# Kernel tuning notes

Hardware: AMD Instinct MI355X
Metric: run time of the kernel (lower is better)

Reference implementation:

```python
import jax, jax.numpy as jnp
import numpy as np

GROUPS = 32
EPS = 1e-5


def group_norm(x, gamma, beta):
    B, C, D, H, W = x.shape
    xr = x.reshape(B, GROUPS, C // GROUPS, D, H, W)
    mean = xr.mean(axis=(2, 3, 4, 5), keepdims=True)
    var = xr.var(axis=(2, 3, 4, 5), keepdims=True)
    xn = (xr - mean) * jax.lax.rsqrt(var + EPS)
    xn = xn.reshape(B, C, D, H, W)
    return xn * gamma[None, :, None, None, None] + beta[None, :, None, None, None]


def conv1x1(h, w, b):
    # 1x1x1 Conv3d == channel matmul. w: [O, C], b: [O]
    return jnp.einsum('oc,bcdhw->bodhw', w, h) + b[None, :, None, None, None]


def setup_inputs() -> dict:
    key = jax.random.key(0)
    ks = jax.random.split(key, 10)
    B, C, D, H, W = 2, 128, 16, 16, 16
    x = jax.random.normal(ks[0], (B, C, D, H, W), dtype=jnp.float32)
    gn_w = jnp.ones((C,), dtype=jnp.float32)
    gn_b = jnp.zeros((C,), dtype=jnp.float32)
    # xavier_uniform for [C, C, 1, 1, 1] conv: fan_in = fan_out = C
    lim = float(np.sqrt(6.0 / (C + C)))
    wq = jax.random.uniform(ks[1], (C, C), jnp.float32, -lim, lim)
    wk = jax.random.uniform(ks[2], (C, C), jnp.float32, -lim, lim)
    wv = jax.random.uniform(ks[3], (C, C), jnp.float32, -lim, lim)
    wp = jax.random.uniform(ks[4], (C, C), jnp.float32, -lim, lim) * 1e-05
    bq = jnp.zeros((C,), jnp.float32)
    bk = jnp.zeros((C,), jnp.float32)
    bv = jnp.zeros((C,), jnp.float32)
    bp = jnp.zeros((C,), jnp.float32)
    return {"x": x, "gn_w": gn_w, "gn_b": gn_b, "wq": wq, "bq": bq,
            "wk": wk, "bk": bk, "wv": wv, "bv": bv, "wp": wp, "bp": bp}


def reference(x, gn_w, gn_b, wq, bq, wk, bk, wv, bv, wp, bp):
    B, C, D, H, W = x.shape
    N = D * H * W
    h = group_norm(x, gn_w, gn_b)
    q = conv1x1(h, wq, bq)
    k = conv1x1(h, wk, bk)
    v = conv1x1(h, wv, bv)
    q = q.transpose(0, 2, 3, 4, 1).reshape(B, N, C)   # [B, N, C]
    k = k.reshape(B, C, N)                            # [B, C, N]
    v = v.transpose(0, 2, 3, 4, 1).reshape(B, N, C)   # [B, N, C]
    w = jnp.einsum('bnc,bcm->bnm', q, k) * (C ** -0.5)  # [B, N, N]
    w = jax.nn.softmax(w, axis=-1)
    h = jnp.einsum('bnm,bmc->bnc', w, v)              # [B, N, C]
    h = h.reshape(B, D, H, W, C).transpose(0, 4, 1, 2, 3)
    h = conv1x1(h, wp, bp)
    return x + h
```

## Files before the change

kernel.cpp:

```cpp
#include <hip/hip_runtime.h>
#include <math.h>

#define CC 128
#define NN 4096
#define BB 2
#define NGROUPS 32
#define CPG 4
#define GSIZE (CPG*NN)
#define KSPLIT 8

typedef __attribute__((ext_vector_type(8))) __bf16 bf16x8;
typedef __attribute__((ext_vector_type(4))) float floatx4;

__device__ __forceinline__ unsigned short f2bf(float f) {
  union { float f; unsigned u; } v; v.f = f;
  unsigned r = v.u + 0x7fff + ((v.u >> 16) & 1);
  return (unsigned short)(r >> 16);
}
__device__ __forceinline__ float bf2f(unsigned short u) {
  return __uint_as_float(((unsigned)u) << 16);
}


__device__ __forceinline__ void stage_tile(const unsigned short* __restrict__ gtile,
                                           unsigned short* ltile, int w, int lane) {
  int swl = ((lane >> 2) << 5) | ((((lane & 3) ^ ((lane >> 3) & 3))) << 3);
  #pragma unroll
  for (int j = 0; j < 4; j++) {
    int off = (w*4 + j) * 512;
    __builtin_amdgcn_global_load_lds(
        (const __attribute__((address_space(1))) unsigned int*)(gtile + off + swl),
        (__attribute__((address_space(3))) unsigned int*)(ltile + off),
        16, 0, 0);
  }
}

__global__ void gn_stats_kernel(const float* __restrict__ x, float2* __restrict__ stats,
                                const float* __restrict__ wq, const float* __restrict__ wk,
                                const float* __restrict__ wv, const float* __restrict__ wp,
                                unsigned short* __restrict__ wqb, unsigned short* __restrict__ wkb,
                                unsigned short* __restrict__ wvb, unsigned short* __restrict__ wpb) {
  int t = threadIdx.x;
  if (blockIdx.x < 256) {
    int bid = blockIdx.x;
    const float4* base = (const float4*)(x + (size_t)bid * 4096);
    float4 v = base[t];
    float s  = v.x + v.y + v.z + v.w;
    float ss = v.x*v.x + v.y*v.y + v.z*v.z + v.w*v.w;
    #pragma unroll
    for (int off = 1; off < 64; off <<= 1) {
      s  += __shfl_xor(s, off);
      ss += __shfl_xor(ss, off);
    }
    __shared__ float sred[4], ssred[4];
    if ((t & 63) == 0) { sred[t >> 6] = s; ssred[t >> 6] = ss; }
    __syncthreads();
    if (t == 0)
      stats[bid] = make_float2(sred[0]+sred[1]+sred[2]+sred[3],
                               ssred[0]+ssred[1]+ssred[2]+ssred[3]);
  } else {
    const float sc = 0.08838834764831845f;
    int i = (blockIdx.x - 256) * 256 + t;
    int id = i >> 12, local = i & 4095;
    const float* src = id==0 ? wq : id==1 ? wk : id==2 ? wv : wp;
    unsigned short* dst = id==0 ? wqb : id==1 ? wkb : id==2 ? wvb : wpb;
    float s = (id == 0) ? sc : 1.0f;
    float4 v = ((const float4*)src)[local];
    unsigned p0 = (unsigned)f2bf(v.x*s) | ((unsigned)f2bf(v.y*s) << 16);
    unsigned p1 = (unsigned)f2bf(v.z*s) | ((unsigned)f2bf(v.w*s) << 16);
    ((uint2*)dst)[local] = make_uint2(p0, p1);
  }
}

__global__ __launch_bounds__(256, 2) void qkv_kernel(
    const float* __restrict__ x, const float2* __restrict__ stats,
    const float* __restrict__ gamma, const float* __restrict__ beta,
    const unsigned short* __restrict__ wqb, const unsigned short* __restrict__ wkb,
    const unsigned short* __restrict__ wvb,
    const float* __restrict__ bq, const float* __restrict__ bk, const float* __restrict__ bv,
    unsigned short* __restrict__ q, unsigned short* __restrict__ k, unsigned short* __restrict__ v) {
  int b = blockIdx.y, n0 = blockIdx.x * 16;
  __shared__ unsigned short hs[16][130];
  __shared__ unsigned short vs[16][136];
  __shared__ float gm[NGROUPS], gr[NGROUPS], aa[CC], ab[CC];
  int t = threadIdx.x;
  if (t < NGROUPS) {
    float su = 0.f, ssq = 0.f;
    #pragma unroll
    for (int j = 0; j < 4; j++) {
      float2 p = stats[(b*NGROUPS + t)*4 + j];
      su += p.x; ssq += p.y;
    }
    float mean = su * (1.0f/GSIZE);
    float var  = ssq * (1.0f/GSIZE) - mean*mean;
    gm[t] = mean;
    gr[t] = rsqrtf(var + 1e-5f);
  }
  __syncthreads();
  if (t < CC) {
    int g = t >> 2;
    float a = gr[g] * gamma[t];
    aa[t] = a;
    ab[t] = beta[t] - gm[g] * a;
  }
  __syncthreads();
  #pragma unroll
  for (int j = 0; j < 2; j++) {
    int idx = j*256 + t;
    int c = idx >> 2, n4 = idx & 3;
    float4 xv = *(const float4*)(x + ((size_t)b*CC + c)*NN + n0 + n4*4);
    float a = aa[c], bc = ab[c];
    hs[n4*4+0][c] = f2bf(a*xv.x + bc);
    hs[n4*4+1][c] = f2bf(a*xv.y + bc);
    hs[n4*4+2][c] = f2bf(a*xv.z + bc);
    hs[n4*4+3][c] = f2bf(a*xv.w + bc);
  }
  __syncthreads();
  int w = t >> 6, lane = t & 63, quad = lane >> 4, c = lane & 15;
  int o0 = w * 32;
  bf16x8 af[4];
  #pragma unroll
  for (int ks = 0; ks < 4; ks++)
    af[ks] = *(const bf16x8*)&hs[c][ks*32 + quad*8];
  floatx4 aq[2], ak[2], av[2];
  #pragma unroll
  for (int ct = 0; ct < 2; ct++) {
    aq[ct] = (floatx4){0.f,0.f,0.f,0.f};
    ak[ct] = (floatx4){0.f,0.f,0.f,0.f};
    av[ct] = (floatx4){0.f,0.f,0.f,0.f};
  }
  #pragma unroll
  for (int ks = 0; ks < 4; ks++) {
    #pragma unroll
    for (int ct = 0; ct < 2; ct++) {
      size_t woff = (size_t)(o0 + ct*16 + c)*CC + ks*32 + quad*8;
      bf16x8 bq8 = *(const bf16x8*)(wqb + woff);
      bf16x8 bk8 = *(const bf16x8*)(wkb + woff);
      bf16x8 bv8 = *(const bf16x8*)(wvb + woff);
      aq[ct] = __builtin_amdgcn_mfma_f32_16x16x32_bf16(af[ks], bq8, aq[ct], 0, 0, 0);
      ak[ct] = __builtin_amdgcn_mfma_f32_16x16x32_bf16(af[ks], bk8, ak[ct], 0, 0, 0);
      av[ct] = __builtin_amdgcn_mfma_f32_16x16x32_bf16(af[ks], bv8, av[ct], 0, 0, 0);
    }
  }
  {
    const float sc = 0.08838834764831845f;
    size_t base = (size_t)b*NN*CC + (size_t)blockIdx.x*2048 + w*512;
    #pragma unroll
    for (int ct = 0; ct < 2; ct++) {
      float bqi = bq[o0 + ct*16 + c] * sc;
      float bki = bk[o0 + ct*16 + c];
      #pragma unroll
      for (int r = 0; r < 4; r++) {
        int idx = (quad*4 + r)*32 + ct*16 + c;
        q[base + idx] = f2bf(aq[ct][r] + bqi);
        k[base + idx] = f2bf(ak[ct][r] + bki);
      }
    }
  }
  #pragma unroll
  for (int ct = 0; ct < 2; ct++) {
    float bvi = bv[o0 + ct*16 + c];
    #pragma unroll
    for (int r = 0; r < 4; r++)
      vs[quad*4 + r][o0 + ct*16 + c] = f2bf(av[ct][r] + bvi);
  }
  __syncthreads();
  {
    int ch = t >> 1, part = t & 1;
    int mbase = (n0 & 16) + part*8;
    unsigned pk[4];
    #pragma unroll
    for (int j = 0; j < 4; j++) {
      unsigned lo = vs[part*8 + j*2    ][ch];
      unsigned hi = vs[part*8 + j*2 + 1][ch];
      pk[j] = lo | (hi << 16);
    }
    *(uint4*)(v + (size_t)b*NN*CC + ((size_t)(n0 >> 5))*4096 + (ch >> 4)*512
              + (ch & 15)*32 + mbase) = make_uint4(pk[0], pk[1], pk[2], pk[3]);
  }
}

__global__ __launch_bounds__(256, 2) void attn_kernel(
    const unsigned short* __restrict__ qm,
    const unsigned short* __restrict__ km,
    const unsigned short* __restrict__ vm,
    unsigned short* __restrict__ Opart,
    float* __restrict__ lpart) {
  int b    = blockIdx.z;
  int kh   = blockIdx.y;
  int t    = threadIdx.x;
  int w    = t >> 6, lane = t & 63, quad = lane >> 4, c = lane & 15;

  __shared__ unsigned short Kbuf[8192];
  __shared__ unsigned short Vbuf[8192];
  __shared__ unsigned short Pl[4][32][88];

  int fragoff = c*32 + quad*8;
  int kvoff   = (c << 5) | (((quad ^ ((c >> 1) & 3))) << 3);

  bf16x8 qa[2][4];
  const unsigned short* qbase = qm + (size_t)b*NN*CC + ((size_t)(blockIdx.x*8 + w*2))*2048;
  #pragma unroll
  for (int rt = 0; rt < 2; rt++)
    #pragma unroll
    for (int ks = 0; ks < 4; ks++)
      qa[rt][ks] = *(const bf16x8*)(qbase + rt*2048 + ks*512 + fragoff);

  floatx4 O[2][8];
  #pragma unroll
  for (int rt = 0; rt < 2; rt++)
    #pragma unroll
    for (int ct = 0; ct < 8; ct++) O[rt][ct] = (floatx4){0.f,0.f,0.f,0.f};
  float lsum[2] = {0.f, 0.f};

  const unsigned short* kt0 = km + (size_t)b*NN*CC + (size_t)kh*(NN/KSPLIT)*CC;
  const unsigned short* vt0 = vm + (size_t)b*NN*CC + (size_t)kh*(NN/KSPLIT)*CC;

  const int ITERS = NN/KSPLIT/64;

  stage_tile(kt0, Kbuf, w, lane);
  stage_tile(vt0, Vbuf, w, lane);
  __syncthreads();

  for (int it = 0; it < ITERS; it++) {
    floatx4 ST[2][4];
    #pragma unroll
    for (int rt = 0; rt < 2; rt++)
      #pragma unroll
      for (int ct = 0; ct < 4; ct++) ST[rt][ct] = (floatx4){0.f,0.f,0.f,0.f};
    #pragma unroll
    for (int ks = 0; ks < 4; ks++) {
      #pragma unroll
      for (int ct = 0; ct < 4; ct++) {
        bf16x8 kf = *(const bf16x8*)&Kbuf[ct*2048 + ks*512 + kvoff];
        ST[0][ct] = __builtin_amdgcn_mfma_f32_16x16x32_bf16(kf, qa[0][ks], ST[0][ct], 0, 0, 0);
        ST[1][ct] = __builtin_amdgcn_mfma_f32_16x16x32_bf16(kf, qa[1][ks], ST[1][ct], 0, 0, 0);
      }
    }
    #pragma unroll
    for (int rt = 0; rt < 2; rt++) {
      #pragma unroll
      for (int ct = 0; ct < 4; ct++) {
        float e0 = __expf(ST[rt][ct][0]);
        float e1 = __expf(ST[rt][ct][1]);
        float e2 = __expf(ST[rt][ct][2]);
        float e3 = __expf(ST[rt][ct][3]);
        lsum[rt] += (e0 + e1) + (e2 + e3);
        unsigned p01 = (__float_as_uint(e1) & 0xffff0000u) | (__float_as_uint(e0) >> 16);
        unsigned p23 = (__float_as_uint(e3) & 0xffff0000u) | (__float_as_uint(e2) >> 16);
        *(uint2*)&Pl[w][rt*16 + c][ct*16 + quad*4] = make_uint2(p01, p23);
      }
    }
    __syncthreads();
    if (it+1 < ITERS) stage_tile(kt0 + (size_t)(it+1)*8192, Kbuf, w, lane);
    #pragma unroll
    for (int ks2 = 0; ks2 < 2; ks2++) {
      bf16x8 pa0 = *(const bf16x8*)(&Pl[w][c     ][ks2*32 + quad*8]);
      bf16x8 pa1 = *(const bf16x8*)(&Pl[w][16 + c][ks2*32 + quad*8]);
      #pragma unroll
      for (int ct = 0; ct < 8; ct++) {
        bf16x8 vf = *(const bf16x8*)&Vbuf[ks2*4096 + ct*512 + kvoff];
        O[0][ct] = __builtin_amdgcn_mfma_f32_16x16x32_bf16(pa0, vf, O[0][ct], 0, 0, 0);
        O[1][ct] = __builtin_amdgcn_mfma_f32_16x16x32_bf16(pa1, vf, O[1][ct], 0, 0, 0);
      }
    }
    __syncthreads();
    if (it+1 < ITERS) stage_tile(vt0 + (size_t)(it+1)*8192, Vbuf, w, lane);
  }

  size_t nbase = (size_t)(kh*BB + b)*NN + blockIdx.x*128 + w*32;
  #pragma unroll
  for (int rt = 0; rt < 2; rt++) {
    float vsum = lsum[rt];
    vsum += __shfl_xor(vsum, 16);
    vsum += __shfl_xor(vsum, 32);
    if (lane < 16) lpart[nbase + rt*16 + lane] = vsum;
  }
  bool odd = (c & 1);
  int colpair = (c & ~1);
  #pragma unroll
  for (int rt = 0; rt < 2; rt++) {
    #pragma unroll
    for (int ct = 0; ct < 8; ct++) {
      unsigned u0 = f2bf(O[rt][ct][0]);
      unsigned u1 = f2bf(O[rt][ct][1]);
      unsigned u2 = f2bf(O[rt][ct][2]);
      unsigned u3 = f2bf(O[rt][ct][3]);
      unsigned s01 = odd ? u0 : u1;
      unsigned g01 = __shfl_xor((int)s01, 1);
      unsigned p0 = odd ? (g01 | (u1 << 16)) : (u0 | (g01 << 16));
      unsigned s23 = odd ? u2 : u3;
      unsigned g23 = __shfl_xor((int)s23, 1);
      unsigned p1 = odd ? (g23 | (u3 << 16)) : (u2 | (g23 << 16));
      int rowA = rt*16 + quad*4 + (odd ? 1 : 0);
      int rowB = rt*16 + quad*4 + (odd ? 3 : 2);
      *(unsigned*)(Opart + (nbase + rowA)*CC + ct*16 + colpair) = p0;
      *(unsigned*)(Opart + (nbase + rowB)*CC + ct*16 + colpair) = p1;
    }
  }
}

__global__ __launch_bounds__(256, 2) void combine_kernel(
    const unsigned short* __restrict__ Opart, const float* __restrict__ lpart,
    const unsigned short* __restrict__ wpb, const float* __restrict__ bp,
    const float* __restrict__ x, float* __restrict__ out) {
  int b = blockIdx.y, n0 = blockIdx.x * 16;
  int t = threadIdx.x;
  __shared__ unsigned short hs[16][130];
  __shared__ float ps[16][132];
  __shared__ float linv[16];
  if (t < 16) {
    float l = 0.f;
    #pragma unroll
    for (int kh = 0; kh < KSPLIT; kh++)
      l += lpart[((size_t)(kh*BB + b))*NN + n0 + t];
    linv[t] = 1.f / l;
  }
  __syncthreads();
  {
    int n = t >> 4, ch0 = (t & 15) * 8;
    float acc[8];
    #pragma unroll
    for (int j = 0; j < 8; j++) acc[j] = 0.f;
    #pragma unroll
    for (int kh = 0; kh < KSPLIT; kh++) {
      uint4 a = *(const uint4*)(Opart + ((size_t)(kh*BB + b)*NN + n0 + n)*CC + ch0);
      unsigned uu[4] = {a.x, a.y, a.z, a.w};
      #pragma unroll
      for (int j = 0; j < 4; j++) {
        acc[j*2    ] += bf2f((unsigned short)(uu[j] & 0xffff));
        acc[j*2 + 1] += bf2f((unsigned short)(uu[j] >> 16));
      }
    }
    float li = linv[n];
    #pragma unroll
    for (int j = 0; j < 8; j++) hs[n][ch0 + j] = f2bf(acc[j] * li);
  }
  __syncthreads();
  int w = t >> 6, lane = t & 63, quad = lane >> 4, c = lane & 15;
  int o0 = w * 32;
  floatx4 acc[2];
  #pragma unroll
  for (int ct = 0; ct < 2; ct++) acc[ct] = (floatx4){0.f,0.f,0.f,0.f};
  #pragma unroll
  for (int ks = 0; ks < 4; ks++) {
    bf16x8 af = *(const bf16x8*)&hs[c][ks*32 + quad*8];
    #pragma unroll
    for (int ct = 0; ct < 2; ct++) {
      bf16x8 bfr = *(const bf16x8*)(wpb + (size_t)(o0 + ct*16 + c)*CC + ks*32 + quad*8);
      acc[ct] = __builtin_amdgcn_mfma_f32_16x16x32_bf16(af, bfr, acc[ct], 0, 0, 0);
    }
  }
  #pragma unroll
  for (int ct = 0; ct < 2; ct++)
    #pragma unroll
    for (int r = 0; r < 4; r++)
      ps[quad*4 + r][o0 + ct*16 + c] = acc[ct][r];
  __syncthreads();
  int o = t >> 1, nh = (t & 1) * 8;
  float bi = bp[o];
  const float* xr = x + ((size_t)b*CC + o)*NN + n0 + nh;
  float* orow = out + ((size_t)b*CC + o)*NN + n0 + nh;
  #pragma unroll
  for (int j4 = 0; j4 < 2; j4++) {
    float4 xv = ((const float4*)xr)[j4];
    float4 ov;
    ov.x = xv.x + ps[nh + j4*4 + 0][o] + bi;
    ov.y = xv.y + ps[nh + j4*4 + 1][o] + bi;
    ov.z = xv.z + ps[nh + j4*4 + 2][o] + bi;
    ov.w = xv.w + ps[nh + j4*4 + 3][o] + bi;
    ((float4*)orow)[j4] = ov;
  }
}

extern "C" void kernel_launch(void* const* d_in, const int* in_sizes, int n_in,
                              void* d_out, int out_size, void* d_ws, size_t ws_size,
                              hipStream_t stream) {
  const float* x    = (const float*)d_in[0];
  const float* gn_w = (const float*)d_in[1];
  const float* gn_b = (const float*)d_in[2];
  const float* wq   = (const float*)d_in[3];
  const float* bq   = (const float*)d_in[4];
  const float* wk   = (const float*)d_in[5];
  const float* bk   = (const float*)d_in[6];
  const float* wv   = (const float*)d_in[7];
  const float* bv   = (const float*)d_in[8];
  const float* wp   = (const float*)d_in[9];
  const float* bp   = (const float*)d_in[10];
  float* out = (float*)d_out;

  char* ws = (char*)d_ws;
  float2*         stats = (float2*)(ws);
  unsigned short* wqb   = (unsigned short*)(ws + 8192);
  unsigned short* wkb   = (unsigned short*)(ws + 8192 + 32768);
  unsigned short* wvb   = (unsigned short*)(ws + 8192 + 65536);
  unsigned short* wpb   = (unsigned short*)(ws + 8192 + 98304);
  unsigned short* qb    = (unsigned short*)(ws + 262144);
  unsigned short* kb    = (unsigned short*)(ws + 262144 + 2097152);
  unsigned short* vb    = (unsigned short*)(ws + 262144 + 2*2097152);
  unsigned short* Opart = (unsigned short*)(ws + 6553600);
  float*          lpart = (float*)(ws + 6553600 + 16777216);

  gn_stats_kernel<<<dim3(320), 256, 0, stream>>>(x, stats, wq, wk, wv, wp,
                                                 wqb, wkb, wvb, wpb);
  qkv_kernel     <<<dim3(NN/16, BB), 256, 0, stream>>>(x, stats, gn_w, gn_b,
                                                       wqb, wkb, wvb, bq, bk, bv,
                                                       qb, kb, vb);
  attn_kernel    <<<dim3(NN/128, KSPLIT, BB), 256, 0, stream>>>(qb, kb, vb, Opart, lpart);
  combine_kernel <<<dim3(NN/16, BB), 256, 0, stream>>>(Opart, lpart, wpb, bp, x, out);
}
```

Before: 116.5 us.

## Fuse four kernels into one cooperative kernel with grid-wide syncs

```diff
diff --git a/kernel.cpp b/kernel.cpp
--- a/kernel.cpp
+++ b/kernel.cpp
@@ -1,5 +1,8 @@
 #include <hip/hip_runtime.h>
+#include <hip/hip_cooperative_groups.h>
 #include <math.h>
+
+namespace cg = cooperative_groups;
 
 #define CC 128
 #define NN 4096
@@ -32,6 +35,341 @@
         (const __attribute__((address_space(1))) unsigned int*)(gtile + off + swl),
         (__attribute__((address_space(3))) unsigned int*)(ltile + off),
         16, 0, 0);
+  }
+}
+
+struct S1 { float sred[4]; float ssred[4]; };
+struct S2 { unsigned short hs[16][130]; unsigned short vs[16][136];
+            float gm[NGROUPS]; float gr[NGROUPS]; float aa[CC]; float ab[CC]; };
+struct S3 { unsigned short Kbuf[8192]; unsigned short Vbuf[8192];
+            unsigned short Pl[4][32][88]; };
+struct S4 { unsigned short hs[16][130]; float ps[16][132]; float linv[16]; };
+union SharedU { S1 s1; S2 s2; S3 s3; S4 s4; };
+
+__global__ __launch_bounds__(256, 2) void fused_kernel(
+    const float* __restrict__ x, const float* __restrict__ gamma, const float* __restrict__ beta,
+    const float* __restrict__ wq, const float* __restrict__ bq,
+    const float* __restrict__ wk, const float* __restrict__ bk,
+    const float* __restrict__ wv, const float* __restrict__ bv,
+    const float* __restrict__ wp, const float* __restrict__ bp,
+    float2* __restrict__ stats,
+    unsigned short* __restrict__ wqb, unsigned short* __restrict__ wkb,
+    unsigned short* __restrict__ wvb, unsigned short* __restrict__ wpb,
+    unsigned short* __restrict__ qb, unsigned short* __restrict__ kb,
+    unsigned short* __restrict__ vb,
+    unsigned short* __restrict__ Opart, float* __restrict__ lpart,
+    float* __restrict__ out) {
+  cg::grid_group grid = cg::this_grid();
+  __shared__ SharedU su;
+  const int bid = blockIdx.x;
+  const int t   = threadIdx.x;
+
+  if (bid < 256) {
+    const float4* base = (const float4*)(x + (size_t)bid * 4096);
+    float4 v = base[t];
+    float s  = v.x + v.y + v.z + v.w;
+    float ss = v.x*v.x + v.y*v.y + v.z*v.z + v.w*v.w;
+    #pragma unroll
+    for (int off = 1; off < 64; off <<= 1) {
+      s  += __shfl_xor(s, off);
+      ss += __shfl_xor(ss, off);
+    }
+    if ((t & 63) == 0) { su.s1.sred[t >> 6] = s; su.s1.ssred[t >> 6] = ss; }
+    __syncthreads();
+    if (t == 0)
+      stats[bid] = make_float2(su.s1.sred[0]+su.s1.sred[1]+su.s1.sred[2]+su.s1.sred[3],
+                               su.s1.ssred[0]+su.s1.ssred[1]+su.s1.ssred[2]+su.s1.ssred[3]);
+  } else if (bid < 320) {
+    const float sc = 0.08838834764831845f;
+    int i = (bid - 256) * 256 + t;
+    int id = i >> 12, local = i & 4095;
+    const float* src = id==0 ? wq : id==1 ? wk : id==2 ? wv : wp;
+    unsigned short* dst = id==0 ? wqb : id==1 ? wkb : id==2 ? wvb : wpb;
+    float s = (id == 0) ? sc : 1.0f;
+    float4 v = ((const float4*)src)[local];
+    unsigned p0 = (unsigned)f2bf(v.x*s) | ((unsigned)f2bf(v.y*s) << 16);
+    unsigned p1 = (unsigned)f2bf(v.z*s) | ((unsigned)f2bf(v.w*s) << 16);
+    ((uint2*)dst)[local] = make_uint2(p0, p1);
+  }
+  __threadfence();
+  grid.sync();
+
+  {
+    int b = bid >> 8, bx = bid & 255, n0 = bx * 16;
+    if (t < NGROUPS) {
+      float su_=0.f, ssq=0.f;
+      #pragma unroll
+      for (int j = 0; j < 4; j++) {
+        float2 p = stats[(b*NGROUPS + t)*4 + j];
+        su_ += p.x; ssq += p.y;
+      }
+      float mean = su_ * (1.0f/GSIZE);
+      float var  = ssq * (1.0f/GSIZE) - mean*mean;
+      su.s2.gm[t] = mean;
+      su.s2.gr[t] = rsqrtf(var + 1e-5f);
+    }
+    __syncthreads();
+    if (t < CC) {
+      int g = t >> 2;
+      float a = su.s2.gr[g] * gamma[t];
+      su.s2.aa[t] = a;
+      su.s2.ab[t] = beta[t] - su.s2.gm[g] * a;
+    }
+    __syncthreads();
+    #pragma unroll
+    for (int j = 0; j < 2; j++) {
+      int idx = j*256 + t;
+      int c = idx >> 2, n4 = idx & 3;
+      float4 xv = *(const float4*)(x + ((size_t)b*CC + c)*NN + n0 + n4*4);
+      float a = su.s2.aa[c], bc = su.s2.ab[c];
+      su.s2.hs[n4*4+0][c] = f2bf(a*xv.x + bc);
+      su.s2.hs[n4*4+1][c] = f2bf(a*xv.y + bc);
+      su.s2.hs[n4*4+2][c] = f2bf(a*xv.z + bc);
+      su.s2.hs[n4*4+3][c] = f2bf(a*xv.w + bc);
+    }
+    __syncthreads();
+    int w = t >> 6, lane = t & 63, quad = lane >> 4, c = lane & 15;
+    int o0 = w * 32;
+    bf16x8 af[4];
+    #pragma unroll
+    for (int ks = 0; ks < 4; ks++)
+      af[ks] = *(const bf16x8*)&su.s2.hs[c][ks*32 + quad*8];
+    floatx4 aq[2], ak[2], av[2];
+    #pragma unroll
+    for (int ct = 0; ct < 2; ct++) {
+      aq[ct] = (floatx4){0.f,0.f,0.f,0.f};
+      ak[ct] = (floatx4){0.f,0.f,0.f,0.f};
+      av[ct] = (floatx4){0.f,0.f,0.f,0.f};
+    }
+    #pragma unroll
+    for (int ks = 0; ks < 4; ks++) {
+      #pragma unroll
+      for (int ct = 0; ct < 2; ct++) {
+        size_t woff = (size_t)(o0 + ct*16 + c)*CC + ks*32 + quad*8;
+        bf16x8 bq8 = *(const bf16x8*)(wqb + woff);
+        bf16x8 bk8 = *(const bf16x8*)(wkb + woff);
+        bf16x8 bv8 = *(const bf16x8*)(wvb + woff);
+        aq[ct] = __builtin_amdgcn_mfma_f32_16x16x32_bf16(af[ks], bq8, aq[ct], 0, 0, 0);
+        ak[ct] = __builtin_amdgcn_mfma_f32_16x16x32_bf16(af[ks], bk8, ak[ct], 0, 0, 0);
+        av[ct] = __builtin_amdgcn_mfma_f32_16x16x32_bf16(af[ks], bv8, av[ct], 0, 0, 0);
+      }
+    }
+    {
+      const float sc = 0.08838834764831845f;
+      size_t base = (size_t)b*NN*CC + (size_t)bx*2048 + w*512;
+      #pragma unroll
+      for (int ct = 0; ct < 2; ct++) {
+        float bqi = bq[o0 + ct*16 + c] * sc;
+        float bki = bk[o0 + ct*16 + c];
+        #pragma unroll
+        for (int r = 0; r < 4; r++) {
+          int idx = (quad*4 + r)*32 + ct*16 + c;
+          qb[base + idx] = f2bf(aq[ct][r] + bqi);
+          kb[base + idx] = f2bf(ak[ct][r] + bki);
+        }
+      }
+    }
+    #pragma unroll
+    for (int ct = 0; ct < 2; ct++) {
+      float bvi = bv[o0 + ct*16 + c];
+      #pragma unroll
+      for (int r = 0; r < 4; r++)
+        su.s2.vs[quad*4 + r][o0 + ct*16 + c] = f2bf(av[ct][r] + bvi);
+    }
+    __syncthreads();
+    {
+      int ch = t >> 1, part = t & 1;
+      int mbase = (n0 & 16) + part*8;
+      unsigned pk[4];
+      #pragma unroll
+      for (int j = 0; j < 4; j++) {
+        unsigned lo = su.s2.vs[part*8 + j*2    ][ch];
+        unsigned hi = su.s2.vs[part*8 + j*2 + 1][ch];
+        pk[j] = lo | (hi << 16);
+      }
+      *(uint4*)(vb + (size_t)b*NN*CC + ((size_t)(n0 >> 5))*4096 + (ch >> 4)*512
+                + (ch & 15)*32 + mbase) = make_uint4(pk[0], pk[1], pk[2], pk[3]);
+    }
+  }
+  __threadfence();
+  grid.sync();
+
+  {
+    int b  = bid >> 8;
+    int kh = (bid >> 5) & 7;
+    int bx = bid & 31;
+    int w = t >> 6, lane = t & 63, quad = lane >> 4, c = lane & 15;
+    int fragoff = c*32 + quad*8;
+    int kvoff   = (c << 5) | (((quad ^ ((c >> 1) & 3))) << 3);
+
+    bf16x8 qa[2][4];
+    const unsigned short* qbase = qb + (size_t)b*NN*CC + ((size_t)(bx*8 + w*2))*2048;
+    #pragma unroll
+    for (int rt = 0; rt < 2; rt++)
+      #pragma unroll
+      for (int ks = 0; ks < 4; ks++)
+        qa[rt][ks] = *(const bf16x8*)(qbase + rt*2048 + ks*512 + fragoff);
+
+    floatx4 O[2][8];
+    #pragma unroll
+    for (int rt = 0; rt < 2; rt++)
+      #pragma unroll
+      for (int ct = 0; ct < 8; ct++) O[rt][ct] = (floatx4){0.f,0.f,0.f,0.f};
+    float lsum[2] = {0.f, 0.f};
+
+    const unsigned short* kt0 = kb + (size_t)b*NN*CC + (size_t)kh*(NN/KSPLIT)*CC;
+    const unsigned short* vt0 = vb + (size_t)b*NN*CC + (size_t)kh*(NN/KSPLIT)*CC;
+
+    const int ITERS = NN/KSPLIT/64;
+
+    stage_tile(kt0, su.s3.Kbuf, w, lane);
+    stage_tile(vt0, su.s3.Vbuf, w, lane);
+    __syncthreads();
+
+    for (int it = 0; it < ITERS; it++) {
+      floatx4 ST[2][4];
+      #pragma unroll
+      for (int rt = 0; rt < 2; rt++)
+        #pragma unroll
+        for (int ct = 0; ct < 4; ct++) ST[rt][ct] = (floatx4){0.f,0.f,0.f,0.f};
+      #pragma unroll
+      for (int ks = 0; ks < 4; ks++) {
+        #pragma unroll
+        for (int ct = 0; ct < 4; ct++) {
+          bf16x8 kf = *(const bf16x8*)&su.s3.Kbuf[ct*2048 + ks*512 + kvoff];
+          ST[0][ct] = __builtin_amdgcn_mfma_f32_16x16x32_bf16(kf, qa[0][ks], ST[0][ct], 0, 0, 0);
+          ST[1][ct] = __builtin_amdgcn_mfma_f32_16x16x32_bf16(kf, qa[1][ks], ST[1][ct], 0, 0, 0);
+        }
+      }
+      #pragma unroll
+      for (int rt = 0; rt < 2; rt++) {
+        #pragma unroll
+        for (int ct = 0; ct < 4; ct++) {
+          float e0 = __expf(ST[rt][ct][0]);
+          float e1 = __expf(ST[rt][ct][1]);
+          float e2 = __expf(ST[rt][ct][2]);
+          float e3 = __expf(ST[rt][ct][3]);
+          lsum[rt] += (e0 + e1) + (e2 + e3);
+          unsigned p01 = (__float_as_uint(e1) & 0xffff0000u) | (__float_as_uint(e0) >> 16);
+          unsigned p23 = (__float_as_uint(e3) & 0xffff0000u) | (__float_as_uint(e2) >> 16);
+          *(uint2*)&su.s3.Pl[w][rt*16 + c][ct*16 + quad*4] = make_uint2(p01, p23);
+        }
+      }
+      __syncthreads();
+      if (it+1 < ITERS) stage_tile(kt0 + (size_t)(it+1)*8192, su.s3.Kbuf, w, lane);
+      #pragma unroll
+      for (int ks2 = 0; ks2 < 2; ks2++) {
+        bf16x8 pa0 = *(const bf16x8*)(&su.s3.Pl[w][c     ][ks2*32 + quad*8]);
+        bf16x8 pa1 = *(const bf16x8*)(&su.s3.Pl[w][16 + c][ks2*32 + quad*8]);
+        #pragma unroll
+        for (int ct = 0; ct < 8; ct++) {
+          bf16x8 vf = *(const bf16x8*)&su.s3.Vbuf[ks2*4096 + ct*512 + kvoff];
+          O[0][ct] = __builtin_amdgcn_mfma_f32_16x16x32_bf16(pa0, vf, O[0][ct], 0, 0, 0);
+          O[1][ct] = __builtin_amdgcn_mfma_f32_16x16x32_bf16(pa1, vf, O[1][ct], 0, 0, 0);
+        }
+      }
+      __syncthreads();
+      if (it+1 < ITERS) stage_tile(vt0 + (size_t)(it+1)*8192, su.s3.Vbuf, w, lane);
+    }
+
+    size_t nbase = (size_t)(kh*BB + b)*NN + bx*128 + w*32;
+    #pragma unroll
+    for (int rt = 0; rt < 2; rt++) {
+      float vsum = lsum[rt];
+      vsum += __shfl_xor(vsum, 16);
+      vsum += __shfl_xor(vsum, 32);
+      if (lane < 16) lpart[nbase + rt*16 + lane] = vsum;
+    }
+    bool odd = (c & 1);
+    int colpair = (c & ~1);
+    #pragma unroll
+    for (int rt = 0; rt < 2; rt++) {
+      #pragma unroll
+      for (int ct = 0; ct < 8; ct++) {
+        unsigned u0 = f2bf(O[rt][ct][0]);
+        unsigned u1 = f2bf(O[rt][ct][1]);
+        unsigned u2 = f2bf(O[rt][ct][2]);
+        unsigned u3 = f2bf(O[rt][ct][3]);
+        unsigned s01 = odd ? u0 : u1;
+        unsigned g01 = __shfl_xor((int)s01, 1);
+        unsigned p0 = odd ? (g01 | (u1 << 16)) : (u0 | (g01 << 16));
+        unsigned s23 = odd ? u2 : u3;
+        unsigned g23 = __shfl_xor((int)s23, 1);
+        unsigned p1 = odd ? (g23 | (u3 << 16)) : (u2 | (g23 << 16));
+        int rowA = rt*16 + quad*4 + (odd ? 1 : 0);
+        int rowB = rt*16 + quad*4 + (odd ? 3 : 2);
+        *(unsigned*)(Opart + (nbase + rowA)*CC + ct*16 + colpair) = p0;
+        *(unsigned*)(Opart + (nbase + rowB)*CC + ct*16 + colpair) = p1;
+      }
+    }
+  }
+  __threadfence();
+  grid.sync();
+
+  {
+    int b = bid >> 8, n0 = (bid & 255) * 16;
+    if (t < 16) {
+      float l = 0.f;
+      #pragma unroll
+      for (int kh = 0; kh < KSPLIT; kh++)
+        l += lpart[((size_t)(kh*BB + b))*NN + n0 + t];
+      su.s4.linv[t] = 1.f / l;
+    }
+    __syncthreads();
+    {
+      int n = t >> 4, ch0 = (t & 15) * 8;
+      float acc[8];
+      #pragma unroll
+      for (int j = 0; j < 8; j++) acc[j] = 0.f;
+      #pragma unroll
+      for (int kh = 0; kh < KSPLIT; kh++) {
+        uint4 a = *(const uint4*)(Opart + ((size_t)(kh*BB + b)*NN + n0 + n)*CC + ch0);
+        unsigned uu[4] = {a.x, a.y, a.z, a.w};
+        #pragma unroll
+        for (int j = 0; j < 4; j++) {
+          acc[j*2    ] += bf2f((unsigned short)(uu[j] & 0xffff));
+          acc[j*2 + 1] += bf2f((unsigned short)(uu[j] >> 16));
+        }
+      }
+      float li = su.s4.linv[n];
+      #pragma unroll
+      for (int j = 0; j < 8; j++) su.s4.hs[n][ch0 + j] = f2bf(acc[j] * li);
+    }
+    __syncthreads();
+    int w = t >> 6, lane = t & 63, quad = lane >> 4, c = lane & 15;
+    int o0 = w * 32;
+    floatx4 acc[2];
+    #pragma unroll
+    for (int ct = 0; ct < 2; ct++) acc[ct] = (floatx4){0.f,0.f,0.f,0.f};
+    #pragma unroll
+    for (int ks = 0; ks < 4; ks++) {
+      bf16x8 af = *(const bf16x8*)&su.s4.hs[c][ks*32 + quad*8];
+      #pragma unroll
+      for (int ct = 0; ct < 2; ct++) {
+        bf16x8 bfr = *(const bf16x8*)(wpb + (size_t)(o0 + ct*16 + c)*CC + ks*32 + quad*8);
+        acc[ct] = __builtin_amdgcn_mfma_f32_16x16x32_bf16(af, bfr, acc[ct], 0, 0, 0);
+      }
+    }
+    #pragma unroll
+    for (int ct = 0; ct < 2; ct++)
+      #pragma unroll
+      for (int r = 0; r < 4; r++)
+        su.s4.ps[quad*4 + r][o0 + ct*16 + c] = acc[ct][r];
+    __syncthreads();
+    int o = t >> 1, nh = (t & 1) * 8;
+    float bi = bp[o];
+    const float* xr = x + ((size_t)b*CC + o)*NN + n0 + nh;
+    float* orow = out + ((size_t)b*CC + o)*NN + n0 + nh;
+    #pragma unroll
+    for (int j4 = 0; j4 < 2; j4++) {
+      float4 xv = ((const float4*)xr)[j4];
+      float4 ov;
+      ov.x = xv.x + su.s4.ps[nh + j4*4 + 0][o] + bi;
+      ov.y = xv.y + su.s4.ps[nh + j4*4 + 1][o] + bi;
+      ov.z = xv.z + su.s4.ps[nh + j4*4 + 2][o] + bi;
+      ov.w = xv.w + su.s4.ps[nh + j4*4 + 3][o] + bi;
+      ((float4*)orow)[j4] = ov;
+    }
   }
 }
 
@@ -181,11 +519,9 @@
 }
 
 __global__ __launch_bounds__(256, 2) void attn_kernel(
-    const unsigned short* __restrict__ qm,
-    const unsigned short* __restrict__ km,
+    const unsigned short* __restrict__ qm, const unsigned short* __restrict__ km,
     const unsigned short* __restrict__ vm,
-    unsigned short* __restrict__ Opart,
-    float* __restrict__ lpart) {
+    unsigned short* __restrict__ Opart, float* __restrict__ lpart) {
   int b    = blockIdx.z;
   int kh   = blockIdx.y;
   int t    = threadIdx.x;
@@ -401,11 +737,24 @@
   unsigned short* Opart = (unsigned short*)(ws + 6553600);
   float*          lpart = (float*)(ws + 6553600 + 16777216);
 
-  gn_stats_kernel<<<dim3(320), 256, 0, stream>>>(x, stats, wq, wk, wv, wp,
-                                                 wqb, wkb, wvb, wpb);
-  qkv_kernel     <<<dim3(NN/16, BB), 256, 0, stream>>>(x, stats, gn_w, gn_b,
-                                                       wqb, wkb, wvb, bq, bk, bv,
-                                                       qb, kb, vb);
-  attn_kernel    <<<dim3(NN/128, KSPLIT, BB), 256, 0, stream>>>(qb, kb, vb, Opart, lpart);
-  combine_kernel <<<dim3(NN/16, BB), 256, 0, stream>>>(Opart, lpart, wpb, bp, x, out);
-}
+  void* kargs[] = {
+    (void*)&x, (void*)&gn_w, (void*)&gn_b,
+    (void*)&wq, (void*)&bq, (void*)&wk, (void*)&bk,
+    (void*)&wv, (void*)&bv, (void*)&wp, (void*)&bp,
+    (void*)&stats, (void*)&wqb, (void*)&wkb, (void*)&wvb, (void*)&wpb,
+    (void*)&qb, (void*)&kb, (void*)&vb,
+    (void*)&Opart, (void*)&lpart, (void*)&out
+  };
+  hipError_t err = hipLaunchCooperativeKernel((const void*)fused_kernel,
+                                              dim3(512), dim3(256),
+                                              kargs, 0, stream);
+  if (err != hipSuccess) {
+    gn_stats_kernel<<<dim3(320), 256, 0, stream>>>(x, stats, wq, wk, wv, wp,
+                                                   wqb, wkb, wvb, wpb);
+    qkv_kernel     <<<dim3(NN/16, BB), 256, 0, stream>>>(x, stats, gn_w, gn_b,
+                                                         wqb, wkb, wvb, bq, bk, bv,
+                                                         qb, kb, vb);
+    attn_kernel    <<<dim3(NN/128, KSPLIT, BB), 256, 0, stream>>>(qb, kb, vb, Opart, lpart);
+    combine_kernel <<<dim3(NN/16, BB), 256, 0, stream>>>(Opart, lpart, wpb, bp, x, out);
+  }
+}
```

Result: slower. 464.3 us (+298.4%).

## Double-buffer K tiles, load V directly to registers, use exp2 softmax

Applied to the files above, without the earlier changes.

```diff
diff --git a/kernel.cpp b/kernel.cpp
--- a/kernel.cpp
+++ b/kernel.cpp
@@ -59,7 +59,7 @@
       stats[bid] = make_float2(sred[0]+sred[1]+sred[2]+sred[3],
                                ssred[0]+ssred[1]+ssred[2]+ssred[3]);
   } else {
-    const float sc = 0.08838834764831845f;
+    const float sc = 0.1275174389522736f;
     int i = (blockIdx.x - 256) * 256 + t;
     int id = i >> 12, local = i & 4095;
     const float* src = id==0 ? wq : id==1 ? wk : id==2 ? wv : wp;
@@ -143,7 +143,7 @@
     }
   }
   {
-    const float sc = 0.08838834764831845f;
+    const float sc = 0.1275174389522736f;
     size_t base = (size_t)b*NN*CC + (size_t)blockIdx.x*2048 + w*512;
     #pragma unroll
     for (int ct = 0; ct < 2; ct++) {
@@ -191,8 +191,7 @@
   int t    = threadIdx.x;
   int w    = t >> 6, lane = t & 63, quad = lane >> 4, c = lane & 15;
 
-  __shared__ unsigned short Kbuf[8192];
-  __shared__ unsigned short Vbuf[8192];
+  __shared__ unsigned short Kbuf[2][8192];
   __shared__ unsigned short Pl[4][32][88];
 
   int fragoff = c*32 + quad*8;
@@ -218,11 +217,18 @@
 
   const int ITERS = NN/KSPLIT/64;
 
-  stage_tile(kt0, Kbuf, w, lane);
-  stage_tile(vt0, Vbuf, w, lane);
+  stage_tile(kt0, Kbuf[0], w, lane);
   __syncthreads();
 
   for (int it = 0; it < ITERS; it++) {
+    const unsigned short* Kb = Kbuf[it & 1];
+    bf16x8 vreg[2][8];
+    #pragma unroll
+    for (int ks2 = 0; ks2 < 2; ks2++)
+      #pragma unroll
+      for (int ct = 0; ct < 8; ct++)
+        vreg[ks2][ct] = *(const bf16x8*)(vt0 + (size_t)it*8192 + ks2*4096 + ct*512 + fragoff);
+    if (it+1 < ITERS) stage_tile(kt0 + (size_t)(it+1)*8192, Kbuf[(it+1) & 1], w, lane);
     floatx4 ST[2][4];
     #pragma unroll
     for (int rt = 0; rt < 2; rt++)
@@ -232,7 +238,7 @@
     for (int ks = 0; ks < 4; ks++) {
       #pragma unroll
       for (int ct = 0; ct < 4; ct++) {
-        bf16x8 kf = *(const bf16x8*)&Kbuf[ct*2048 + ks*512 + kvoff];
+        bf16x8 kf = *(const bf16x8*)&Kb[ct*2048 + ks*512 + kvoff];
         ST[0][ct] = __builtin_amdgcn_mfma_f32_16x16x32_bf16(kf, qa[0][ks], ST[0][ct], 0, 0, 0);
         ST[1][ct] = __builtin_amdgcn_mfma_f32_16x16x32_bf16(kf, qa[1][ks], ST[1][ct], 0, 0, 0);
       }
@@ -241,31 +247,27 @@
     for (int rt = 0; rt < 2; rt++) {
       #pragma unroll
       for (int ct = 0; ct < 4; ct++) {
-        float e0 = __expf(ST[rt][ct][0]);
-        float e1 = __expf(ST[rt][ct][1]);
-        float e2 = __expf(ST[rt][ct][2]);
-        float e3 = __expf(ST[rt][ct][3]);
+        float e0 = exp2f(ST[rt][ct][0]);
+        float e1 = exp2f(ST[rt][ct][1]);
+        float e2 = exp2f(ST[rt][ct][2]);
+        float e3 = exp2f(ST[rt][ct][3]);
         lsum[rt] += (e0 + e1) + (e2 + e3);
         unsigned p01 = (__float_as_uint(e1) & 0xffff0000u) | (__float_as_uint(e0) >> 16);
         unsigned p23 = (__float_as_uint(e3) & 0xffff0000u) | (__float_as_uint(e2) >> 16);
         *(uint2*)&Pl[w][rt*16 + c][ct*16 + quad*4] = make_uint2(p01, p23);
       }
     }
-    __syncthreads();
-    if (it+1 < ITERS) stage_tile(kt0 + (size_t)(it+1)*8192, Kbuf, w, lane);
     #pragma unroll
     for (int ks2 = 0; ks2 < 2; ks2++) {
       bf16x8 pa0 = *(const bf16x8*)(&Pl[w][c     ][ks2*32 + quad*8]);
       bf16x8 pa1 = *(const bf16x8*)(&Pl[w][16 + c][ks2*32 + quad*8]);
       #pragma unroll
       for (int ct = 0; ct < 8; ct++) {
-        bf16x8 vf = *(const bf16x8*)&Vbuf[ks2*4096 + ct*512 + kvoff];
-        O[0][ct] = __builtin_amdgcn_mfma_f32_16x16x32_bf16(pa0, vf, O[0][ct], 0, 0, 0);
-        O[1][ct] = __builtin_amdgcn_mfma_f32_16x16x32_bf16(pa1, vf, O[1][ct], 0, 0, 0);
+        O[0][ct] = __builtin_amdgcn_mfma_f32_16x16x32_bf16(pa0, vreg[ks2][ct], O[0][ct], 0, 0, 0);
+        O[1][ct] = __builtin_amdgcn_mfma_f32_16x16x32_bf16(pa1, vreg[ks2][ct], O[1][ct], 0, 0, 0);
       }
     }
     __syncthreads();
-    if (it+1 < ITERS) stage_tile(vt0 + (size_t)(it+1)*8192, Vbuf, w, lane);
   }
 
   size_t nbase = (size_t)(kh*BB + b)*NN + blockIdx.x*128 + w*32;
```

Result: slower. 126.0 us (+8.1%).
